# Optimization experiments

Measured on AMD Instinct MI355X. Metric: run time of the kernel, lower is better.

## Reference

```python
import jax, jax.numpy as jnp
import numpy as np

B, S, D, H, F, E = 4, 1024, 1024, 16, 4096, 8
HD = D // H  # head dim


def setup_inputs() -> dict:
    key = jax.random.key(0)
    ks = jax.random.split(key, 8)
    p = lambda k, shp: jax.random.normal(k, shp, jnp.float32) * 0.02
    return {
        "x": jax.random.normal(ks[0], (B, S, D), jnp.float32),
        "mask": jnp.ones((B, S), jnp.int32),
        "in_proj_w": p(ks[1], (3 * D, D)),
        "in_proj_b": jnp.zeros((3 * D,), jnp.float32),
        "out_proj_w": p(ks[2], (D, D)),
        "out_proj_b": jnp.zeros((D,), jnp.float32),
        "ln1_g": jnp.ones((D,), jnp.float32),
        "ln1_b": jnp.zeros((D,), jnp.float32),
        "ln2_g": jnp.ones((D,), jnp.float32),
        "ln2_b": jnp.zeros((D,), jnp.float32),
        "gate_w": p(ks[3], (E, D)),
        "gate_b": jnp.zeros((E,), jnp.float32),
        "w1": p(ks[4], (E, F, D)),
        "b1": jnp.zeros((E, F), jnp.float32),
        "w2": p(ks[5], (E, D, F)),
        "b2": jnp.zeros((E, D), jnp.float32),
    }


def _layernorm(x, g, b, eps=1e-5):
    m = x.mean(-1, keepdims=True)
    v = ((x - m) ** 2).mean(-1, keepdims=True)
    return (x - m) / jnp.sqrt(v + eps) * g + b


def _mha(x, key_pad, in_proj_w, in_proj_b, out_proj_w, out_proj_b):
    # combined QKV projection as in torch nn.MultiheadAttention
    qkv = x @ in_proj_w.T + in_proj_b  # (B,S,3D)
    q, k, v = jnp.split(qkv, 3, axis=-1)
    def heads(t):
        return t.reshape(B, S, H, HD).transpose(0, 2, 1, 3)  # (B,H,S,HD)
    q, k, v = heads(q), heads(k), heads(v)
    scores = jnp.einsum("bhqd,bhkd->bhqk", q, k) / jnp.sqrt(jnp.float32(HD))
    scores = jnp.where(key_pad[:, None, None, :], -1e30, scores)
    attn = jax.nn.softmax(scores, axis=-1)
    out = jnp.einsum("bhqk,bhkd->bhqd", attn, v)  # (B,H,S,HD)
    out = out.transpose(0, 2, 1, 3).reshape(B, S, D)
    return out @ out_proj_w.T + out_proj_b


def _moe(x, gate_w, gate_b, w1, b1, w2, b2):
    logits = x @ gate_w.T + gate_b            # (B,S,E)
    probs = jax.nn.softmax(logits, axis=-1)
    # dense all-expert FFN (faithful to original: every expert computed)
    h = jax.nn.relu(jnp.einsum("bsd,efd->bsef", x, w1) + b1)   # (B,S,E,F)
    all_out = jnp.einsum("bsef,edf->bsed", h, w2) + b2          # (B,S,E,D)
    top_vals, top_idx = jax.lax.top_k(probs, 2)                 # (B,S,2)
    weights = top_vals / (top_vals.sum(-1, keepdims=True) + 1e-9)
    sel = jnp.take_along_axis(all_out, top_idx[..., None], axis=2)  # (B,S,2,D)
    return (sel * weights[..., None]).sum(axis=2)


def reference(x, mask, in_proj_w, in_proj_b, out_proj_w, out_proj_b,
              ln1_g, ln1_b, ln2_g, ln2_b, gate_w, gate_b, w1, b1, w2, b2):
    key_pad = mask == 0  # (B,S) bool
    attn_out = _mha(x, key_pad, in_proj_w, in_proj_b, out_proj_w, out_proj_b)
    x1 = _layernorm(x + attn_out, ln1_g, ln1_b)
    ff = _moe(x1, gate_w, gate_b, w1, b1, w2, b2)
    return _layernorm(x1 + ff, ln2_g, ln2_b)
```

## Files before the change

### kernel.cpp

```cpp
#include <hip/hip_runtime.h>

typedef __attribute__((ext_vector_type(8))) short bf16x8;
typedef __attribute__((ext_vector_type(4))) float f32x4;

#define DEV __device__ __forceinline__

static constexpr int Bb = 4, Sq = 1024, Dd = 1024, Hh = 16, HDd = 64, Ff = 4096, Ee = 8;
static constexpr int Nn = Bb * Sq;
static constexpr int TD = 3 * Dd;
static constexpr int PMAX = 2 * Nn + Ee * 256;

DEV unsigned short f2bf(float x) {
  union { float f; unsigned u; } c; c.f = x;
  unsigned r = c.u + 0x7FFFu + ((c.u >> 16) & 1u);
  return (unsigned short)(r >> 16);
}

typedef const __attribute__((address_space(1))) unsigned int* gas_t;
typedef __attribute__((address_space(3))) unsigned int* las_t;
DEV void gload16(const void* g, void* l) {
  __builtin_amdgcn_global_load_lds((gas_t)g, (las_t)l, 16, 0, 0);
}

__global__ __launch_bounds__(256) void cvt_kernel(const float* __restrict__ in,
                                                  unsigned short* __restrict__ out) {
  int i = blockIdx.x * 256 + threadIdx.x;
  const float4 a = *(const float4*)(in + (size_t)i * 8);
  const float4 b = *(const float4*)(in + (size_t)i * 8 + 4);
  union { uint4 u; unsigned short s[8]; } pk;
  pk.s[0] = f2bf(a.x); pk.s[1] = f2bf(a.y); pk.s[2] = f2bf(a.z); pk.s[3] = f2bf(a.w);
  pk.s[4] = f2bf(b.x); pk.s[5] = f2bf(b.y); pk.s[6] = f2bf(b.z); pk.s[7] = f2bf(b.w);
  *(uint4*)(out + (size_t)i * 8) = pk.u;
}

DEV void xcd_swz(int& bx, int& by, int gx, int gy) {
  const int nwg = gx * gy;
  int orig = by * gx + bx;
  int q = nwg >> 3, r = nwg & 7;
  int xcd = orig & 7, lin = orig >> 3;
  int wg = (xcd < r ? xcd * (q + 1) : r * (q + 1) + (xcd - r) * q) + lin;
  bx = wg / gy; by = wg % gy;
}

__global__ __launch_bounds__(512) void gemm8p_up(
    const unsigned short* __restrict__ A, const unsigned short* __restrict__ Bw,
    const float* __restrict__ bias, unsigned short* __restrict__ o0,
    const int* __restrict__ poff) {
  constexpr int K = Dd;
  constexpr int NT = K / 64;
  int bx = blockIdx.x, by = blockIdx.y;
  xcd_swz(bx, by, gridDim.x, gridDim.y);
  const int m0 = bx * 256;
  if (m0 >= poff[Ee]) return;
  int e = 0;
#pragma unroll
  for (int k = 1; k < Ee; ++k) if (m0 >= poff[k]) e = k;
  const int n0 = by * 256;
  const unsigned short* Bptr = Bw + (size_t)e * Ff * K;
  const float* biasptr = bias + e * Ff;

  __shared__ __align__(128) unsigned short As[2 * 256 * 64];
  __shared__ __align__(128) unsigned short Bs[2 * 256 * 64];

  const int tid = threadIdx.x;
  const int lane = tid & 63, wid = tid >> 6;
  const int aw = wid & 1, bw = wid >> 1;
  const int lr = lane & 15, lk = lane >> 4;

  const char* aS[2][2]; const char* bS[2][2]; int dOf[2];
#pragma unroll
  for (int it = 0; it < 2; ++it) {
    int b = it * 8192 + tid * 16;
    int r = b >> 7;
    int colb = (b & 127) ^ ((r & 7) << 4);
#pragma unroll
    for (int h = 0; h < 2; ++h) {
      aS[h][it] = (const char*)(A + (size_t)(m0 + h * 128 + r) * K) + colb;
      bS[h][it] = (const char*)(Bptr + (size_t)(n0 + h * 128 + r) * K) + colb;
    }
    dOf[it] = it * 8192 + wid * 1024;
  }
  int aO[2][2][4], bO[2][2][2];
#pragma unroll
  for (int h = 0; h < 2; ++h)
#pragma unroll
    for (int ks = 0; ks < 2; ++ks) {
#pragma unroll
      for (int mi = 0; mi < 4; ++mi) {
        int ra = h * 128 + aw * 64 + mi * 16 + lr;
        aO[h][ks][mi] = ra * 64 + (((ks * 4 + lk) ^ (ra & 7)) << 3);
      }
#pragma unroll
      for (int ni = 0; ni < 2; ++ni) {
        int rb = h * 128 + bw * 32 + ni * 16 + lr;
        bO[h][ks][ni] = rb * 64 + (((ks * 4 + lk) ^ (rb & 7)) << 3);
      }
    }

  f32x4 acc[4][4][2] = {};

  auto ST_A = [&](int t, int h) {
    int buf = t & 1;
#pragma unroll
    for (int it = 0; it < 2; ++it)
      gload16(aS[h][it] + (size_t)t * 128, (char*)As + buf * 32768 + h * 16384 + dOf[it]);
  };
  auto ST_B = [&](int t, int h) {
    int buf = t & 1;
#pragma unroll
    for (int it = 0; it < 2; ++it)
      gload16(bS[h][it] + (size_t)t * 128, (char*)Bs + buf * 32768 + h * 16384 + dOf[it]);
  };

  ST_A(0, 0); ST_B(0, 0); ST_B(0, 1); ST_A(0, 1);

  for (int t = 0; t < NT; ++t) {
    const unsigned short* Ab = As + (t & 1) * 16384;
    const unsigned short* Bb = Bs + (t & 1) * 16384;
#pragma unroll
    for (int p = 0; p < 4; ++p) {
      const int ah = p >> 1, bh = p & 1;
      if (t + 1 < NT) {
        if (p == 0)      ST_A(t + 1, 0);
        else if (p == 1) ST_B(t + 1, 0);
        else if (p == 2) ST_B(t + 1, 1);
        else             ST_A(t + 1, 1);
        asm volatile("s_waitcnt vmcnt(6)" ::: "memory");
      } else {
        if (p == 0)      asm volatile("s_waitcnt vmcnt(4)" ::: "memory");
        else if (p == 1) asm volatile("s_waitcnt vmcnt(2)" ::: "memory");
        else             asm volatile("s_waitcnt vmcnt(0)" ::: "memory");
      }
      __builtin_amdgcn_sched_barrier(0);
      asm volatile("s_barrier" ::: "memory");
      __builtin_amdgcn_sched_barrier(0);
      bf16x8 af[2][4], bf[2][2];
#pragma unroll
      for (int ks = 0; ks < 2; ++ks) {
#pragma unroll
        for (int mi = 0; mi < 4; ++mi) af[ks][mi] = *(const bf16x8*)&Ab[aO[ah][ks][mi]];
#pragma unroll
        for (int ni = 0; ni < 2; ++ni) bf[ks][ni] = *(const bf16x8*)&Bb[bO[bh][ks][ni]];
      }
      __builtin_amdgcn_s_setprio(1);
#pragma unroll
      for (int ks = 0; ks < 2; ++ks)
#pragma unroll
        for (int mi = 0; mi < 4; ++mi)
#pragma unroll
          for (int ni = 0; ni < 2; ++ni)
            acc[p][mi][ni] = __builtin_amdgcn_mfma_f32_16x16x32_bf16(af[ks][mi], bf[ks][ni], acc[p][mi][ni], 0, 0, 0);
      __builtin_amdgcn_s_setprio(0);
    }
  }

#pragma unroll
  for (int p = 0; p < 4; ++p)
#pragma unroll
    for (int ni = 0; ni < 2; ++ni) {
      const int col = n0 + (p & 1) * 128 + bw * 32 + ni * 16 + lr;
      const float bv = biasptr[col];
#pragma unroll
      for (int mi = 0; mi < 4; ++mi)
#pragma unroll
        for (int i = 0; i < 4; ++i) {
          const int row = m0 + (p >> 1) * 128 + aw * 64 + mi * 16 + lk * 4 + i;
          float v = acc[p][mi][ni][i] + bv;
          o0[(size_t)row * Ff + col] = f2bf(fmaxf(v, 0.f));
        }
    }
}

template <int EPI>
__global__ __launch_bounds__(256) void gemm_bt(
    const unsigned short* __restrict__ A, const unsigned short* __restrict__ Bw,
    const float* __restrict__ bias, void* __restrict__ o0, void* __restrict__ o1,
    void* __restrict__ o2, int M, int Ncols, int K,
    const int* __restrict__ poff) {
  int bx = blockIdx.x, by = blockIdx.y;
  xcd_swz(bx, by, gridDim.x, gridDim.y);
  const int m0 = bx * 128;
  int e = 0;
  if constexpr (EPI == 3) {
    if (m0 >= poff[Ee]) return;
#pragma unroll
    for (int k = 1; k < Ee; ++k) if (m0 >= poff[k]) e = k;
  } else {
    if (m0 >= M) return;
  }
  const int n0 = by * 128;
  const unsigned short* Bptr = Bw + (size_t)e * Ncols * K;
  const float* biasptr = bias + e * Ncols;

  __shared__ __align__(128) unsigned short As[3 * 128 * 32];
  __shared__ __align__(128) unsigned short Bs[3 * 128 * 32];

  const int tid = threadIdx.x;
  const int lane = tid & 63, wid = tid >> 6;
  const int wm = wid >> 1, wn = wid & 1;
  const int lr = lane & 15, lk = lane >> 4;

  const char* aSrc[2]; const char* bSrc[2];
  int dOff[2];
#pragma unroll
  for (int it = 0; it < 2; ++it) {
    int b = it * 4096 + tid * 16;
    int r = b >> 6;
    int colb = (b & 63) ^ (((r >> 1) & 3) << 4);
    aSrc[it] = (const char*)(A + (size_t)(m0 + r) * K) + colb;
    bSrc[it] = (const char*)(Bptr + (size_t)(n0 + r) * K) + colb;
    dOff[it] = it * 4096 + wid * 1024;
  }
  int aOff[4], bOff[4];
#pragma unroll
  for (int i = 0; i < 4; ++i) {
    int ra = wm * 64 + i * 16 + lr;
    aOff[i] = ra * 32 + ((lk ^ ((ra >> 1) & 3)) << 3);
    int rb = wn * 64 + i * 16 + lr;
    bOff[i] = rb * 32 + ((lk ^ ((rb >> 1) & 3)) << 3);
  }

  auto STAGE = [&](int t, int buf) {
#pragma unroll
    for (int it = 0; it < 2; ++it) {
      gload16(aSrc[it] + (size_t)t * 64, (char*)As + buf * 8192 + dOff[it]);
      gload16(bSrc[it] + (size_t)t * 64, (char*)Bs + buf * 8192 + dOff[it]);
    }
  };

  f32x4 acc[4][4] = {};
  const int NT = K >> 5;

  STAGE(0, 0);
  STAGE(1, 1);
  int cb = 0, sb = 2;
  for (int t = 0; t < NT; ++t) {
    if (t + 1 < NT) asm volatile("s_waitcnt vmcnt(4)" ::: "memory");
    else            asm volatile("s_waitcnt vmcnt(0)" ::: "memory");
    __builtin_amdgcn_sched_barrier(0);
    __builtin_amdgcn_s_barrier();
    __builtin_amdgcn_sched_barrier(0);
    if (t + 2 < NT) STAGE(t + 2, sb);
    const unsigned short* Ab = As + cb * 4096;
    const unsigned short* Bb2 = Bs + cb * 4096;
    bf16x8 af[4], bfv[4];
#pragma unroll
    for (int mi = 0; mi < 4; ++mi) af[mi] = *(const bf16x8*)&Ab[aOff[mi]];
#pragma unroll
    for (int ni = 0; ni < 4; ++ni) bfv[ni] = *(const bf16x8*)&Bb2[bOff[ni]];
#pragma unroll
    for (int mi = 0; mi < 4; ++mi)
#pragma unroll
      for (int ni = 0; ni < 4; ++ni)
        acc[mi][ni] = __builtin_amdgcn_mfma_f32_16x16x32_bf16(af[mi], bfv[ni], acc[mi][ni], 0, 0, 0);
    cb = (cb == 2) ? 0 : cb + 1;
    sb = (sb == 2) ? 0 : sb + 1;
  }

#pragma unroll
  for (int ni = 0; ni < 4; ++ni) {
    const int col = n0 + wn * 64 + ni * 16 + lr;
    const float bv = biasptr[col];
#pragma unroll
    for (int mi = 0; mi < 4; ++mi) {
#pragma unroll
      for (int i = 0; i < 4; ++i) {
        const int mloc = wm * 64 + mi * 16 + lk * 4 + i;
        float v = acc[mi][ni][i] + bv;
        if constexpr (EPI == 0) {
          int t = m0 + mloc;
          int which = col >> 10, jj = col & 1023, hh = jj >> 6, hd = jj & 63;
          int bb = t >> 10, s = t & 1023;
          unsigned short* dst = (which == 0) ? (unsigned short*)o0
                              : (which == 1) ? (unsigned short*)o1 : (unsigned short*)o2;
          dst[((size_t)(bb * Hh + hh) * Sq + s) * HDd + hd] = f2bf(v);
        } else if constexpr (EPI == 1) {
          ((float*)o0)[(size_t)(m0 + mloc) * Dd + col] = v;
        } else {
          ((float*)o0)[(size_t)(m0 + mloc) * Dd + col] = v;
        }
      }
    }
  }
}

__global__ __launch_bounds__(256) void attn_kernel(
    const unsigned short* __restrict__ qb, const unsigned short* __restrict__ kb,
    const unsigned short* __restrict__ vb, const int* __restrict__ mask,
    unsigned short* __restrict__ attnb) {
  const int qt = blockIdx.x, h = blockIdx.y, b = blockIdx.z;
  const unsigned short* Q = qb + (size_t)(b * Hh + h) * Sq * HDd;
  const unsigned short* Kg = kb + (size_t)(b * Hh + h) * Sq * HDd;
  const unsigned short* Vg = vb + (size_t)(b * Hh + h) * Sq * HDd;

  __shared__ unsigned short Qs[64 * 72], Ks[64 * 72], Vt[64 * 72], Ps[64 * 72];
  __shared__ float Ssm[64 * 65];
  __shared__ float mS[64], lS[64], aS[64];
  __shared__ int mk[64];

  const int tid = threadIdx.x, lane = tid & 63, wid = tid >> 6;
  const int lr = lane & 15, lk = lane >> 4;

#pragma unroll
  for (int it = 0; it < 2; ++it) {
    int c = tid + it * 256; int r = c >> 3, kc = (c & 7) * 8;
    *(uint4*)&Qs[r * 72 + kc] = *(const uint4*)(Q + (size_t)(qt * 64 + r) * 64 + kc);
  }
  if (tid < 64) { mS[tid] = -1e30f; lS[tid] = 0.f; }

  f32x4 oacc[4] = {};

  for (int kt = 0; kt < 16; ++kt) {
    __syncthreads();
#pragma unroll
    for (int it = 0; it < 2; ++it) {
      int c = tid + it * 256; int r = c >> 3, kc = (c & 7) * 8;
      *(uint4*)&Ks[r * 72 + kc] = *(const uint4*)(Kg + (size_t)(kt * 64 + r) * 64 + kc);
    }
    {
      int kk = tid >> 2, hg = (tid & 3) * 16;
      union { uint4 u[2]; unsigned short s[16]; } tv;
      tv.u[0] = *(const uint4*)(Vg + (size_t)(kt * 64 + kk) * 64 + hg);
      tv.u[1] = *(const uint4*)(Vg + (size_t)(kt * 64 + kk) * 64 + hg + 8);
#pragma unroll
      for (int j = 0; j < 16; ++j) Vt[(hg + j) * 72 + kk] = tv.s[j];
    }
    if (tid < 64) mk[tid] = mask[b * Sq + kt * 64 + tid];
    __syncthreads();

    f32x4 sacc[4] = {};
#pragma unroll
    for (int ks = 0; ks < 2; ++ks) {
      bf16x8 aq = *(const bf16x8*)&Qs[(wid * 16 + lr) * 72 + ks * 32 + lk * 8];
#pragma unroll
      for (int ni = 0; ni < 4; ++ni) {
        bf16x8 bk = *(const bf16x8*)&Ks[(ni * 16 + lr) * 72 + ks * 32 + lk * 8];
        sacc[ni] = __builtin_amdgcn_mfma_f32_16x16x32_bf16(aq, bk, sacc[ni], 0, 0, 0);
      }
    }
#pragma unroll
    for (int ni = 0; ni < 4; ++ni)
#pragma unroll
      for (int i = 0; i < 4; ++i) {
        int r = wid * 16 + lk * 4 + i, cc = ni * 16 + lr;
        float v = sacc[ni][i] * 0.125f;
        if (mk[cc] == 0) v = -1e30f;
        Ssm[r * 65 + cc] = v;
      }
    __syncthreads();
    {
      int r = tid >> 2, cg = (tid & 3) * 16;
      float xv[16];
#pragma unroll
      for (int j = 0; j < 16; ++j) xv[j] = Ssm[r * 65 + cg + j];
      float mx = xv[0];
#pragma unroll
      for (int j = 1; j < 16; ++j) mx = fmaxf(mx, xv[j]);
      mx = fmaxf(mx, __shfl_xor(mx, 1));
      mx = fmaxf(mx, __shfl_xor(mx, 2));
      float mprev = mS[r];
      float mnew = fmaxf(mprev, mx);
      float sum = 0.f;
      union { uint4 u[2]; unsigned short s[16]; } pb;
#pragma unroll
      for (int j = 0; j < 16; ++j) {
        float pv = expf(xv[j] - mnew);
        sum += pv; pb.s[j] = f2bf(pv);
      }
      sum += __shfl_xor(sum, 1);
      sum += __shfl_xor(sum, 2);
      *(uint4*)&Ps[r * 72 + cg] = pb.u[0];
      *(uint4*)&Ps[r * 72 + cg + 8] = pb.u[1];
      if ((tid & 3) == 0) {
        float alpha = expf(mprev - mnew);
        mS[r] = mnew; aS[r] = alpha; lS[r] = lS[r] * alpha + sum;
      }
    }
    __syncthreads();
#pragma unroll
    for (int ni = 0; ni < 4; ++ni)
#pragma unroll
      for (int i = 0; i < 4; ++i)
        oacc[ni][i] *= aS[wid * 16 + lk * 4 + i];
#pragma unroll
    for (int ks = 0; ks < 2; ++ks) {
      bf16x8 ap = *(const bf16x8*)&Ps[(wid * 16 + lr) * 72 + ks * 32 + lk * 8];
#pragma unroll
      for (int ni = 0; ni < 4; ++ni) {
        bf16x8 bv = *(const bf16x8*)&Vt[(ni * 16 + lr) * 72 + ks * 32 + lk * 8];
        oacc[ni] = __builtin_amdgcn_mfma_f32_16x16x32_bf16(ap, bv, oacc[ni], 0, 0, 0);
      }
    }
  }
  __syncthreads();
#pragma unroll
  for (int ni = 0; ni < 4; ++ni)
#pragma unroll
    for (int i = 0; i < 4; ++i) {
      int r = wid * 16 + lk * 4 + i;
      int q = qt * 64 + r;
      float v = oacc[ni][i] / lS[r];
      attnb[((size_t)(b * Sq + q)) * Dd + h * 64 + ni * 16 + lr] = f2bf(v);
    }
}

__global__ __launch_bounds__(256) void ln1_route_kernel(
    const float* __restrict__ a, const float* __restrict__ b2,
    const float* __restrict__ g, const float* __restrict__ beta,
    const float* __restrict__ gw, const float* __restrict__ gb,
    float* __restrict__ outf, unsigned short* __restrict__ outb,
    int* __restrict__ cnt, int* __restrict__ tokslot, float* __restrict__ wtok) {
  const int t = blockIdx.x, tid = threadIdx.x;
  float4 v = *(const float4*)(a + (size_t)t * Dd + tid * 4);
  {
    float4 u = *(const float4*)(b2 + (size_t)t * Dd + tid * 4);
    v.x += u.x; v.y += u.y; v.z += u.z; v.w += u.w;
  }
  const int lane = tid & 63, wid = tid >> 6;
  float s = v.x + v.y + v.z + v.w;
  for (int sh = 1; sh < 64; sh <<= 1) s += __shfl_xor(s, sh);
  __shared__ float red[4], red2[4];
  __shared__ float gred[4 * Ee];
  if (lane == 0) red[wid] = s;
  __syncthreads();
  float mean = (red[0] + red[1] + red[2] + red[3]) * (1.f / Dd);
  float dx = v.x - mean, dy = v.y - mean, dz = v.z - mean, dw = v.w - mean;
  float q = dx * dx + dy * dy + dz * dz + dw * dw;
  for (int sh = 1; sh < 64; sh <<= 1) q += __shfl_xor(q, sh);
  if (lane == 0) red2[wid] = q;
  __syncthreads();
  float var = (red2[0] + red2[1] + red2[2] + red2[3]) * (1.f / Dd);
  float rstd = rsqrtf(var + 1e-5f);
  float4 gg = *(const float4*)(g + tid * 4);
  float4 bbv = *(const float4*)(beta + tid * 4);
  float4 o;
  o.x = dx * rstd * gg.x + bbv.x;
  o.y = dy * rstd * gg.y + bbv.y;
  o.z = dz * rstd * gg.z + bbv.z;
  o.w = dw * rstd * gg.w + bbv.w;
  *(float4*)(outf + (size_t)t * Dd + tid * 4) = o;
  {
    ushort4 pk; pk.x = f2bf(o.x); pk.y = f2bf(o.y); pk.z = f2bf(o.z); pk.w = f2bf(o.w);
    *(ushort4*)(outb + (size_t)t * Dd + tid * 4) = pk;
  }
  float gacc[Ee];
#pragma unroll
  for (int e = 0; e < Ee; ++e) {
    float4 gv = *(const float4*)(gw + (size_t)e * Dd + tid * 4);
    gacc[e] = o.x * gv.x + o.y * gv.y + o.z * gv.z + o.w * gv.w;
  }
#pragma unroll
  for (int e = 0; e < Ee; ++e)
    for (int sh = 1; sh < 64; sh <<= 1) gacc[e] += __shfl_xor(gacc[e], sh);
  if (lane == 0) {
#pragma unroll
    for (int e = 0; e < Ee; ++e) gred[wid * Ee + e] = gacc[e];
  }
  __syncthreads();
  if (tid == 0) {
    float lg[Ee];
#pragma unroll
    for (int e = 0; e < Ee; ++e)
      lg[e] = gred[e] + gred[Ee + e] + gred[2 * Ee + e] + gred[3 * Ee + e] + gb[e];
    float m = lg[0];
#pragma unroll
    for (int e = 1; e < Ee; ++e) m = fmaxf(m, lg[e]);
    float p[Ee], ssum = 0.f;
#pragma unroll
    for (int e = 0; e < Ee; ++e) { p[e] = expf(lg[e] - m); ssum += p[e]; }
    int e0 = 0;
#pragma unroll
    for (int e = 1; e < Ee; ++e) if (p[e] > p[e0]) e0 = e;
    int e1 = -1;
#pragma unroll
    for (int e = 0; e < Ee; ++e) {
      if (e == e0) continue;
      if (e1 < 0 || p[e] > p[e1]) e1 = e;
    }
    float v0 = p[e0] / ssum, v1 = p[e1] / ssum;
    float wsum = v0 + v1 + 1e-9f;
    wtok[t * 2] = v0 / wsum; wtok[t * 2 + 1] = v1 / wsum;
    int p0 = atomicAdd(&cnt[e0], 1);
    tokslot[e0 * Nn + p0] = t * 2;
    int p1 = atomicAdd(&cnt[e1], 1);
    tokslot[e1 * Nn + p1] = t * 2 + 1;
  }
}

__global__ __launch_bounds__(256) void ln2_kernel(
    const float* __restrict__ x1f, const float* __restrict__ ffp,
    const int* __restrict__ inv, const float* __restrict__ wtok,
    const float* __restrict__ g, const float* __restrict__ beta,
    float* __restrict__ out) {
  const int t = blockIdx.x, tid = threadIdx.x;
  const int i0 = inv[2 * t], i1 = inv[2 * t + 1];
  const float w0 = wtok[2 * t], w1 = wtok[2 * t + 1];
  float4 v = *(const float4*)(x1f + (size_t)t * Dd + tid * 4);
  float4 u0 = *(const float4*)(ffp + (size_t)i0 * Dd + tid * 4);
  float4 u1 = *(const float4*)(ffp + (size_t)i1 * Dd + tid * 4);
  v.x += w0 * u0.x + w1 * u1.x; v.y += w0 * u0.y + w1 * u1.y;
  v.z += w0 * u0.z + w1 * u1.z; v.w += w0 * u0.w + w1 * u1.w;
  const int lane = tid & 63, wid = tid >> 6;
  float s = v.x + v.y + v.z + v.w;
  for (int sh = 1; sh < 64; sh <<= 1) s += __shfl_xor(s, sh);
  __shared__ float red[4], red2[4];
  if (lane == 0) red[wid] = s;
  __syncthreads();
  float mean = (red[0] + red[1] + red[2] + red[3]) * (1.f / Dd);
  float dx = v.x - mean, dy = v.y - mean, dz = v.z - mean, dw = v.w - mean;
  float q = dx * dx + dy * dy + dz * dz + dw * dw;
  for (int sh = 1; sh < 64; sh <<= 1) q += __shfl_xor(q, sh);
  if (lane == 0) red2[wid] = q;
  __syncthreads();
  float var = (red2[0] + red2[1] + red2[2] + red2[3]) * (1.f / Dd);
  float rstd = rsqrtf(var + 1e-5f);
  float4 gg = *(const float4*)(g + tid * 4);
  float4 bb = *(const float4*)(beta + tid * 4);
  float4 o;
  o.x = dx * rstd * gg.x + bb.x;
  o.y = dy * rstd * gg.y + bb.y;
  o.z = dz * rstd * gg.z + bb.z;
  o.w = dw * rstd * gg.w + bb.w;
  *(float4*)(out + (size_t)t * Dd + tid * 4) = o;
}

__global__ void offsets_kernel(const int* __restrict__ cnt, int* __restrict__ poff) {
  if (threadIdx.x == 0) {
    int s = 0;
    for (int e = 0; e < Ee; ++e) { poff[e] = s; s += (cnt[e] + 255) & ~255; }
    poff[Ee] = s;
  }
}

__global__ __launch_bounds__(256) void pack_kernel(
    const unsigned short* __restrict__ x1b, const int* __restrict__ tokslot,
    const int* __restrict__ cnt, const int* __restrict__ poff,
    unsigned short* __restrict__ xg, int* __restrict__ inv) {
  const int tid = threadIdx.x;
  const int g = blockIdx.x * 8 + (tid >> 5);
  const int l = tid & 31;
  if (g >= poff[Ee]) return;
  int e = 0;
#pragma unroll
  for (int k = 1; k < Ee; ++k) if (g >= poff[k]) e = k;
  const int pos = g - poff[e];
  uint4* dst = (uint4*)(xg + (size_t)g * Dd);
  if (pos < cnt[e]) {
    const int ent = tokslot[e * Nn + pos];
    if (l == 0) inv[ent] = g;
    const uint4* src = (const uint4*)(x1b + (size_t)(ent >> 1) * Dd);
#pragma unroll
    for (int j = 0; j < 4; ++j) dst[l + j * 32] = src[l + j * 32];
  } else {
    const uint4 z = make_uint4(0, 0, 0, 0);
#pragma unroll
    for (int j = 0; j < 4; ++j) dst[l + j * 32] = z;
  }
}

extern "C" void kernel_launch(void* const* d_in, const int* in_sizes, int n_in,
                              void* d_out, int out_size, void* d_ws, size_t ws_size,
                              hipStream_t stream) {
  const float* x   = (const float*)d_in[0];
  const int*   msk = (const int*)d_in[1];
  const float* ipw = (const float*)d_in[2];
  const float* ipb = (const float*)d_in[3];
  const float* opw = (const float*)d_in[4];
  const float* opb = (const float*)d_in[5];
  const float* g1  = (const float*)d_in[6];
  const float* be1 = (const float*)d_in[7];
  const float* g2  = (const float*)d_in[8];
  const float* be2 = (const float*)d_in[9];
  const float* gw  = (const float*)d_in[10];
  const float* gb  = (const float*)d_in[11];
  const float* w1  = (const float*)d_in[12];
  const float* b1  = (const float*)d_in[13];
  const float* w2  = (const float*)d_in[14];
  const float* b2  = (const float*)d_in[15];
  float* out = (float*)d_out;

  char* p = (char*)d_ws;
  auto carve = [&](size_t bytes) { char* r = p; p += (bytes + 255) & ~(size_t)255; return r; };
  unsigned short* xb   = (unsigned short*)carve((size_t)Nn * Dd * 2);
  unsigned short* qb   = (unsigned short*)carve((size_t)Nn * Dd * 2);
  unsigned short* kb   = (unsigned short*)carve((size_t)Nn * Dd * 2);
  unsigned short* vb   = (unsigned short*)carve((size_t)Nn * Dd * 2);
  float* proj          = (float*)carve((size_t)Nn * Dd * 4);
  float* x1f           = (float*)carve((size_t)Nn * Dd * 4);
  unsigned short* x1b  = (unsigned short*)carve((size_t)Nn * Dd * 2);
  unsigned short* xg   = (unsigned short*)carve((size_t)PMAX * Dd * 2);
  float* ffp           = (float*)carve((size_t)PMAX * Dd * 4);
  unsigned short* hbuf = (unsigned short*)carve((size_t)PMAX * Ff * 2);
  unsigned short* wbuf = (unsigned short*)carve((size_t)Ee * Ff * Dd * 2);
  int* cnt             = (int*)carve(64);
  int* poff            = (int*)carve(64);
  int* tokslot         = (int*)carve((size_t)Ee * Nn * 4);
  float* wtok          = (float*)carve((size_t)2 * Nn * 4);
  int* inv             = (int*)carve((size_t)2 * Nn * 4);
  unsigned short* attnb = xb;

  cvt_kernel<<<Nn * Dd / 2048, 256, 0, stream>>>(x, xb);
  cvt_kernel<<<TD * Dd / 2048, 256, 0, stream>>>(ipw, wbuf);
  gemm_bt<0><<<dim3(Nn / 128, TD / 128), 256, 0, stream>>>(
      xb, wbuf, ipb, qb, kb, vb, Nn, TD, Dd, nullptr);
  attn_kernel<<<dim3(Sq / 64, Hh, Bb), 256, 0, stream>>>(qb, kb, vb, msk, attnb);
  cvt_kernel<<<Dd * Dd / 2048, 256, 0, stream>>>(opw, wbuf);
  gemm_bt<1><<<dim3(Nn / 128, Dd / 128), 256, 0, stream>>>(
      attnb, wbuf, opb, proj, nullptr, nullptr, Nn, Dd, Dd, nullptr);
  hipMemsetAsync(cnt, 0, 64, stream);
  ln1_route_kernel<<<Nn, 256, 0, stream>>>(x, proj, g1, be1, gw, gb,
                                           x1f, x1b, cnt, tokslot, wtok);
  offsets_kernel<<<1, 64, 0, stream>>>(cnt, poff);
  pack_kernel<<<PMAX / 8, 256, 0, stream>>>(x1b, tokslot, cnt, poff, xg, inv);
  cvt_kernel<<<Ee * Ff * Dd / 2048, 256, 0, stream>>>(w1, wbuf);
  gemm8p_up<<<dim3(PMAX / 256, Ff / 256), 512, 0, stream>>>(xg, wbuf, b1, hbuf, poff);
  cvt_kernel<<<Ee * Dd * Ff / 2048, 256, 0, stream>>>(w2, wbuf);
  gemm_bt<3><<<dim3(PMAX / 128, Dd / 128), 256, 0, stream>>>(
      hbuf, wbuf, b2, ffp, nullptr, nullptr, PMAX, Dd, Ff, poff);
  ln2_kernel<<<Nn, 256, 0, stream>>>(x1f, ffp, inv, wtok, g2, be2, out);
}
```

Baseline: 615.1 us.

## Split-K the QKV and output projection GEMMs with separate reduction passes

The QKV projection GEMM is split along K into two halves and the output projection into four, each writing fp32 partials to a scratch buffer that reuses the MoE output buffer. A new combine kernel sums the QKV partials, adds bias, converts to bf16 and scatters into head-major Q/K/V, while the LN1 kernel now sums the four projection partials itself. The aim is more blocks in flight for GEMMs whose grids already have 384 and 256 tiles. The cost is substantial extra fp32 traffic (partials written and reread) plus an additional kernel launch.

```diff
diff --git a/kernel.cpp b/kernel.cpp
--- a/kernel.cpp
+++ b/kernel.cpp
@@ -171,12 +171,13 @@
     }
 }
 
-template <int EPI>
+template <int EPI, int KS = 1>
 __global__ __launch_bounds__(256) void gemm_bt(
     const unsigned short* __restrict__ A, const unsigned short* __restrict__ Bw,
     const float* __restrict__ bias, void* __restrict__ o0, void* __restrict__ o1,
     void* __restrict__ o2, int M, int Ncols, int K,
     const int* __restrict__ poff) {
+  const int kh = (KS > 1) ? blockIdx.z : 0;
   int bx = blockIdx.x, by = blockIdx.y;
   xcd_swz(bx, by, gridDim.x, gridDim.y);
   const int m0 = bx * 128;
@@ -189,6 +190,8 @@
     if (m0 >= M) return;
   }
   const int n0 = by * 128;
+  const int Kloc = K / KS;
+  const int k00 = kh * Kloc;
   const unsigned short* Bptr = Bw + (size_t)e * Ncols * K;
   const float* biasptr = bias + e * Ncols;
 
@@ -207,8 +210,8 @@
     int b = it * 4096 + tid * 16;
     int r = b >> 6;
     int colb = (b & 63) ^ (((r >> 1) & 3) << 4);
-    aSrc[it] = (const char*)(A + (size_t)(m0 + r) * K) + colb;
-    bSrc[it] = (const char*)(Bptr + (size_t)(n0 + r) * K) + colb;
+    aSrc[it] = (const char*)(A + (size_t)(m0 + r) * K + k00) + colb;
+    bSrc[it] = (const char*)(Bptr + (size_t)(n0 + r) * K + k00) + colb;
     dOff[it] = it * 4096 + wid * 1024;
   }
   int aOff[4], bOff[4];
@@ -229,7 +232,7 @@
   };
 
   f32x4 acc[4][4] = {};
-  const int NT = K >> 5;
+  const int NT = Kloc >> 5;
 
   STAGE(0, 0);
   STAGE(1, 1);
@@ -260,7 +263,7 @@
 #pragma unroll
   for (int ni = 0; ni < 4; ++ni) {
     const int col = n0 + wn * 64 + ni * 16 + lr;
-    const float bv = biasptr[col];
+    const float bv = (EPI == 1 && kh == 0) ? biasptr[col] : (EPI == 3 ? biasptr[col] : 0.f);
 #pragma unroll
     for (int mi = 0; mi < 4; ++mi) {
 #pragma unroll
@@ -268,20 +271,39 @@
         const int mloc = wm * 64 + mi * 16 + lk * 4 + i;
         float v = acc[mi][ni][i] + bv;
         if constexpr (EPI == 0) {
-          int t = m0 + mloc;
-          int which = col >> 10, jj = col & 1023, hh = jj >> 6, hd = jj & 63;
-          int bb = t >> 10, s = t & 1023;
-          unsigned short* dst = (which == 0) ? (unsigned short*)o0
-                              : (which == 1) ? (unsigned short*)o1 : (unsigned short*)o2;
-          dst[((size_t)(bb * Hh + hh) * Sq + s) * HDd + hd] = f2bf(v);
+          ((float*)o0)[((size_t)kh * Nn + m0 + mloc) * TD + col] = v;
         } else if constexpr (EPI == 1) {
-          ((float*)o0)[(size_t)(m0 + mloc) * Dd + col] = v;
+          ((float*)o0)[((size_t)kh * Nn + m0 + mloc) * Dd + col] = v;
         } else {
           ((float*)o0)[(size_t)(m0 + mloc) * Dd + col] = v;
         }
       }
     }
   }
+}
+
+__global__ __launch_bounds__(256) void qkv_combine_kernel(
+    const float* __restrict__ tmp, const float* __restrict__ ipb,
+    unsigned short* __restrict__ qb, unsigned short* __restrict__ kb,
+    unsigned short* __restrict__ vb) {
+  const size_t f = ((size_t)blockIdx.x * 256 + threadIdx.x) * 8;
+  const float* t1 = tmp + (size_t)Nn * TD;
+  float4 a0 = *(const float4*)(tmp + f);
+  float4 a1 = *(const float4*)(tmp + f + 4);
+  float4 b0 = *(const float4*)(t1 + f);
+  float4 b1 = *(const float4*)(t1 + f + 4);
+  const int t = (int)(f / TD), col = (int)(f % TD);
+  float4 c0 = *(const float4*)(ipb + col);
+  float4 c1 = *(const float4*)(ipb + col + 4);
+  union { uint4 u; unsigned short s[8]; } pk;
+  pk.s[0] = f2bf(a0.x + b0.x + c0.x); pk.s[1] = f2bf(a0.y + b0.y + c0.y);
+  pk.s[2] = f2bf(a0.z + b0.z + c0.z); pk.s[3] = f2bf(a0.w + b0.w + c0.w);
+  pk.s[4] = f2bf(a1.x + b1.x + c1.x); pk.s[5] = f2bf(a1.y + b1.y + c1.y);
+  pk.s[6] = f2bf(a1.z + b1.z + c1.z); pk.s[7] = f2bf(a1.w + b1.w + c1.w);
+  const int which = col >> 10, jj = col & 1023, hh = jj >> 6, hd = jj & 63;
+  const int bb = t >> 10, s = t & 1023;
+  unsigned short* dst = (which == 0) ? qb : (which == 1) ? kb : vb;
+  *(uint4*)(dst + ((size_t)(bb * Hh + hh) * Sq + s) * HDd + hd) = pk.u;
 }
 
 __global__ __launch_bounds__(256) void attn_kernel(
@@ -405,15 +427,16 @@
 }
 
 __global__ __launch_bounds__(256) void ln1_route_kernel(
-    const float* __restrict__ a, const float* __restrict__ b2,
+    const float* __restrict__ a, const float* __restrict__ proj4,
     const float* __restrict__ g, const float* __restrict__ beta,
     const float* __restrict__ gw, const float* __restrict__ gb,
     float* __restrict__ outf, unsigned short* __restrict__ outb,
     int* __restrict__ cnt, int* __restrict__ tokslot, float* __restrict__ wtok) {
   const int t = blockIdx.x, tid = threadIdx.x;
   float4 v = *(const float4*)(a + (size_t)t * Dd + tid * 4);
-  {
-    float4 u = *(const float4*)(b2 + (size_t)t * Dd + tid * 4);
+#pragma unroll
+  for (int j = 0; j < 4; ++j) {
+    float4 u = *(const float4*)(proj4 + ((size_t)j * Nn + t) * Dd + tid * 4);
     v.x += u.x; v.y += u.y; v.z += u.z; v.w += u.w;
   }
   const int lane = tid & 63, wid = tid >> 6;
@@ -585,7 +608,6 @@
   unsigned short* qb   = (unsigned short*)carve((size_t)Nn * Dd * 2);
   unsigned short* kb   = (unsigned short*)carve((size_t)Nn * Dd * 2);
   unsigned short* vb   = (unsigned short*)carve((size_t)Nn * Dd * 2);
-  float* proj          = (float*)carve((size_t)Nn * Dd * 4);
   float* x1f           = (float*)carve((size_t)Nn * Dd * 4);
   unsigned short* x1b  = (unsigned short*)carve((size_t)Nn * Dd * 2);
   unsigned short* xg   = (unsigned short*)carve((size_t)PMAX * Dd * 2);
@@ -598,24 +620,27 @@
   float* wtok          = (float*)carve((size_t)2 * Nn * 4);
   int* inv             = (int*)carve((size_t)2 * Nn * 4);
   unsigned short* attnb = xb;
+  float* qkvtmp = ffp;
+  float* proj4  = ffp;
 
   cvt_kernel<<<Nn * Dd / 2048, 256, 0, stream>>>(x, xb);
   cvt_kernel<<<TD * Dd / 2048, 256, 0, stream>>>(ipw, wbuf);
-  gemm_bt<0><<<dim3(Nn / 128, TD / 128), 256, 0, stream>>>(
-      xb, wbuf, ipb, qb, kb, vb, Nn, TD, Dd, nullptr);
+  gemm_bt<0, 2><<<dim3(Nn / 128, TD / 128, 2), 256, 0, stream>>>(
+      xb, wbuf, ipb, qkvtmp, nullptr, nullptr, Nn, TD, Dd, nullptr);
+  qkv_combine_kernel<<<Nn * TD / 2048, 256, 0, stream>>>(qkvtmp, ipb, qb, kb, vb);
   attn_kernel<<<dim3(Sq / 64, Hh, Bb), 256, 0, stream>>>(qb, kb, vb, msk, attnb);
   cvt_kernel<<<Dd * Dd / 2048, 256, 0, stream>>>(opw, wbuf);
-  gemm_bt<1><<<dim3(Nn / 128, Dd / 128), 256, 0, stream>>>(
-      attnb, wbuf, opb, proj, nullptr, nullptr, Nn, Dd, Dd, nullptr);
+  gemm_bt<1, 4><<<dim3(Nn / 128, Dd / 128, 4), 256, 0, stream>>>(
+      attnb, wbuf, opb, proj4, nullptr, nullptr, Nn, Dd, Dd, nullptr);
   hipMemsetAsync(cnt, 0, 64, stream);
-  ln1_route_kernel<<<Nn, 256, 0, stream>>>(x, proj, g1, be1, gw, gb,
+  ln1_route_kernel<<<Nn, 256, 0, stream>>>(x, proj4, g1, be1, gw, gb,
                                            x1f, x1b, cnt, tokslot, wtok);
   offsets_kernel<<<1, 64, 0, stream>>>(cnt, poff);
   pack_kernel<<<PMAX / 8, 256, 0, stream>>>(x1b, tokslot, cnt, poff, xg, inv);
   cvt_kernel<<<Ee * Ff * Dd / 2048, 256, 0, stream>>>(w1, wbuf);
   gemm8p_up<<<dim3(PMAX / 256, Ff / 256), 512, 0, stream>>>(xg, wbuf, b1, hbuf, poff);
   cvt_kernel<<<Ee * Dd * Ff / 2048, 256, 0, stream>>>(w2, wbuf);
-  gemm_bt<3><<<dim3(PMAX / 128, Dd / 128), 256, 0, stream>>>(
+  gemm_bt<3, 1><<<dim3(PMAX / 128, Dd / 128), 256, 0, stream>>>(
       hbuf, wbuf, b2, ffp, nullptr, nullptr, PMAX, Dd, Ff, poff);
   ln2_kernel<<<Nn, 256, 0, stream>>>(x1f, ffp, inv, wtok, g2, be2, out);
 }
```

After: 637.7 us. 1.04x slower.
